# Kernel tuning notes

Hardware: AMD Instinct MI355X
Metric: run time of the kernel (lower is better)

Reference implementation:

```python
import jax, jax.numpy as jnp
import numpy as np

K = 3        # kernel_size
STRIDE = 1
PAD = 1
BASIS = 8    # act_fun.get_size()


def cheb_basis(x):
    """Chebyshev polynomial basis T_0..T_{BASIS-1} of tanh(x); appends basis axis."""
    t = jnp.tanh(x)
    polys = [jnp.ones_like(t), t]
    for _ in range(BASIS - 2):
        polys.append(2.0 * t * polys[-1] - polys[-2])
    return jnp.stack(polys, axis=-1)  # (..., BASIS)


def silu(x):
    return x * jax.nn.sigmoid(x)


def unfold(x):
    """torch F.unfold equivalent: (b,c,h,w) -> (b, c, K*K, L), L = ho*wo."""
    b, c, h, w = x.shape
    ho = (h - K + 2 * PAD) // STRIDE + 1
    wo = (w - K + 2 * PAD) // STRIDE + 1
    xp = jnp.pad(x, ((0, 0), (0, 0), (PAD, PAD), (PAD, PAD)))
    pats = [xp[:, :, i:i + STRIDE * ho:STRIDE, j:j + STRIDE * wo:STRIDE]
            for i in range(K) for j in range(K)]
    pats = jnp.stack(pats, axis=2)  # (b, c, K*K, ho, wo)
    return pats.reshape(b, c, K * K, ho * wo), ho, wo


def setup_inputs() -> dict:
    key = jax.random.key(0)
    k1, k2, k3 = jax.random.split(key, 3)
    cin, cout = 64, 64
    x = jax.random.normal(k1, (16, cin, 32, 32), dtype=jnp.float32)
    # xavier_normal_ on (in,out,k^2,1): std = sqrt(2/(fan_in+fan_out)) approx
    w = jax.random.normal(k2, (cin, cout, K * K), dtype=jnp.float32) * jnp.sqrt(2.0 / (cin + cout))
    # normal_(c, 0, 0.1) on (in,out,k^2,1,basis) -> squeeze the broadcast dim
    c = jax.random.normal(k3, (cin, cout, K * K, BASIS), dtype=jnp.float32) * 0.1
    return {"x": x, "w": w, "c": c}


def reference(x, w, c):
    b = x.shape[0]
    pats, ho, wo = unfold(x)          # (b, i, k, l)
    res = silu(pats)                  # residual activation path
    act = cheb_basis(pats)            # (b, i, k, l, s) spline basis
    # sum_i sum_k w[i,o,k] * res[b,i,k,l]
    term1 = jnp.einsum('iok,bikl->bol', w, res)
    # sum_i sum_k sum_s w[i,o,k]*c[i,o,k,s]*act[b,i,k,l,s] (fused, avoids (b,i,o,k,l,s))
    cw = c * w[..., None]             # (i, o, k, s)
    term2 = jnp.einsum('ioks,bikls->bol', cw, act)
    return (term1 + term2).reshape(b, -1, ho, wo)
```

## Files before the change

kernel.cpp:

```cpp
#include <hip/hip_runtime.h>
#include <hip/hip_bf16.h>


#define CIN   64
#define COUT  64
#define HW    32
#define LL    1024
#define NS    8

typedef __attribute__((ext_vector_type(8))) short short8;
typedef __attribute__((ext_vector_type(16))) float f32x16;


__global__ void prep_kernel(const float* __restrict__ w,
                            const float* __restrict__ c,
                            __hip_bfloat16* __restrict__ Wt,
                            float* __restrict__ bias,
                            const float* __restrict__ x,
                            float* __restrict__ dummy) {
    const int bx = blockIdx.x;
    if (bx < 144) {
        const int tid = bx * 256 + threadIdx.x;
        const int i = tid / (9 * COUT);
        const int r = tid - i * 9 * COUT;
        const int k = r / COUT;
        const int o = r - k * COUT;
        const int widx = (i * COUT + o) * 9 + k;
        const float wv = w[widx];
        __hip_bfloat16* dst = Wt + (size_t)tid * NS;
        dst[0] = __float2bfloat16(wv);
#pragma unroll
        for (int s = 1; s < 8; ++s) dst[s] = __float2bfloat16(wv * c[widx * 8 + s]);
        return;
    }
    if (bx < 208) {
        const int o = bx - 144;
        const int i = threadIdx.x;
        if (i >= 64) return;
        float v = 0.f;
#pragma unroll
        for (int k = 0; k < 9; ++k) {
            const int idx = (i * COUT + o) * 9 + k;
            v += w[idx] * c[idx * 8];
        }
#pragma unroll
        for (int off = 32; off > 0; off >>= 1) v += __shfl_down(v, off);
        if (i == 0) bias[o] = v;
        return;
    }
    const int idx = bx - 208;
    const int r  = idx & 7;
    const int m  = idx >> 3;
    const int b  = r + 8 * (m & 1);
    const int ch = m >> 1;
    const float4 v = ((const float4*)(x + (size_t)(b * CIN + ch) * LL))[threadIdx.x];
    const float acc = v.x + v.y + v.z + v.w;
    if (acc == 1.0e-37f) dummy[threadIdx.x] = acc;
}

__global__ __launch_bounds__(1024, 4) void kan_fused_kernel(
        const float* __restrict__ x,
        const __hip_bfloat16* __restrict__ Wt,
        const float* __restrict__ bias,
        float* __restrict__ out) {
    __shared__ __align__(16) unsigned short Wlds[52224];

    const int tid  = threadIdx.x;
    const int wv   = tid >> 6;
    const int lane = tid & 63;
    const int l31  = lane & 31;
    const int half = lane >> 5;
    const int kq   = wv >> 1;
    const int om   = wv & 1;

    const int b    = blockIdx.x;
    const int row0 = blockIdx.y << 1;

    const unsigned short* WtU = (const unsigned short*)Wt;
    float* xf = (float*)Wlds;

#pragma unroll
    for (int p = 0; p < 9; ++p) {
        const int cell = p * 1024 + tid;
        if (cell < 8704) {
            const int ch  = cell / 136;
            const int pos = cell - ch * 136;
            const int r4  = pos / 34;
            const int col = pos - r4 * 34;
            const int gy  = row0 - 1 + r4;
            const int gx  = col - 1;
            float v = 0.f;
            if ((unsigned)gy < 32u && (unsigned)gx < 32u)
                v = x[((size_t)(b * CIN + ch) * HW + gy) * HW + gx];
            xf[cell] = v;
        }
    }
    __syncthreads();

    f32x16 acc0, acc1;
#pragma unroll
    for (int r = 0; r < 16; ++r) { acc0[r] = 0.f; acc1[r] = 0.f; }

    const size_t wlane = ((size_t)(kq * 8 + half) * 9 * 64 + om * 32 + l31) * 8;

    for (int chunk = 0; chunk < 4; ++chunk) {
        unsigned short* ubuf = Wlds + 17408 + (chunk & 1) * 17408;

        auto doCell = [&](int cell) {
            const int kqc = cell / 272;
            const int rr  = cell - kqc * 272;
            const int chl = rr & 1;
            const int pos = rr >> 1;
            const float xv = xf[(kqc * 8 + chunk * 2 + chl) * 136 + pos];
            const float e   = __expf(xv);
            const float sig = e * __builtin_amdgcn_rcpf(1.f + e);
            const float res = xv * sig;
            const float t   = 1.f - 2.f * __builtin_amdgcn_rcpf(__builtin_fmaf(e, e, 1.f));
            const float t2  = t + t;
            const float T2 = __builtin_fmaf(t2, t,  -1.f);
            const float T3 = __builtin_fmaf(t2, T2, -t);
            const float T4 = __builtin_fmaf(t2, T3, -T2);
            const float T5 = __builtin_fmaf(t2, T4, -T3);
            const float T6 = __builtin_fmaf(t2, T5, -T4);
            const float T7 = __builtin_fmaf(t2, T6, -T5);
            union { __hip_bfloat162 h2[4]; float4 f4; } U;
            U.h2[0] = __float22bfloat162_rn(make_float2(res, t));
            U.h2[1] = __float22bfloat162_rn(make_float2(T2, T3));
            U.h2[2] = __float22bfloat162_rn(make_float2(T4, T5));
            U.h2[3] = __float22bfloat162_rn(make_float2(T6, T7));
            *(float4*)(ubuf + cell * 8) = U.f4;
        };
        doCell(tid);
        doCell(tid + 1024);
        if (tid < 128) doCell(tid + 2048);

        __syncthreads();

        const unsigned short* afb = ubuf + kq * 2176;
        const unsigned short* wc  = WtU + wlane + (size_t)chunk * 9216;
#pragma unroll
        for (int kpos = 0; kpos < 9; ++kpos) {
            const int posb = (kpos / 3) * 34 + (kpos % 3);
            short8 af0 = *(const short8*)(afb + ((posb      + l31) * 2 + half) * 8);
            short8 af1 = *(const short8*)(afb + ((posb + 34 + l31) * 2 + half) * 8);
            short8 wf  = *(const short8*)(wc + kpos * 512);
            acc0 = __builtin_amdgcn_mfma_f32_32x32x16_bf16(wf, af0, acc0, 0, 0, 0);
            acc1 = __builtin_amdgcn_mfma_f32_32x32x16_bf16(wf, af1, acc1, 0, 0, 0);
        }
    }

    float* red = (float*)Wlds;
#pragma unroll
    for (int h = 0; h < 2; ++h) {
        if (h) __syncthreads();
        if (om == h) {
#pragma unroll
            for (int r = 0; r < 16; ++r) {
                const int ol = (r & 3) + 8 * (r >> 2) + 4 * half;
                red[(kq * 64 +      l31) * 33 + ol] = acc0[r];
                red[(kq * 64 + 32 + l31) * 33 + ol] = acc1[r];
            }
        }
        __syncthreads();
#pragma unroll
        for (int rep = 0; rep < 2; ++rep) {
            const int v  = rep * 1024 + tid;
            const int p  = v & 63;
            const int ol = v >> 6;
            float s = bias[h * 32 + ol];
#pragma unroll
            for (int kqq = 0; kqq < 8; ++kqq)
                s += red[(kqq * 64 + p) * 33 + ol];
            out[(size_t)(b * COUT + h * 32 + ol) * LL + (row0 + (p >> 5)) * HW + (p & 31)] = s;
        }
    }
}

extern "C" void kernel_launch(void* const* d_in, const int* in_sizes, int n_in,
                              void* d_out, int out_size, void* d_ws, size_t ws_size,
                              hipStream_t stream) {
    const float* x = (const float*)d_in[0];
    const float* w = (const float*)d_in[1];
    const float* c = (const float*)d_in[2];
    float* out = (float*)d_out;

    char* ws = (char*)d_ws;
    __hip_bfloat16* Wt    = (__hip_bfloat16*)(ws);
    float*          bias  = (float*)(ws + 589824);
    float*          dummy = (float*)(ws + 590080);

    prep_kernel<<<1232, 256, 0, stream>>>(w, c, Wt, bias, x, dummy);
    kan_fused_kernel<<<dim3(16, 16), 1024, 0, stream>>>(x, Wt, bias, out);
}
```

Before: 74.92 us.

## Split output channels across blocks and prefetch input per chunk from global

Each block now handles one half of the output channels with 512 threads, doubling the grid, instead of 1024 threads covering both halves. The full x tile is no longer staged in LDS. Each thread loads its cells straight from global memory, prefetching the next chunk's values into registers while the current chunk is processed. The activation buffer layout changes so each half-wave reads contiguous entries, and MFMA issue priority is raised. The basis activations are now computed twice (once per output half), which adds ALU work in exchange for smaller blocks, less LDS and more blocks per device.

```diff
diff --git a/kernel.cpp b/kernel.cpp
--- a/kernel.cpp
+++ b/kernel.cpp
@@ -58,121 +58,129 @@
     if (acc == 1.0e-37f) dummy[threadIdx.x] = acc;
 }
 
-__global__ __launch_bounds__(1024, 4) void kan_fused_kernel(
+__global__ __launch_bounds__(512, 4) void kan_fused_kernel(
         const float* __restrict__ x,
         const __hip_bfloat16* __restrict__ Wt,
         const float* __restrict__ bias,
         float* __restrict__ out) {
-    __shared__ __align__(16) unsigned short Wlds[52224];
+    __shared__ __align__(16) unsigned short Wlds[34816];
 
     const int tid  = threadIdx.x;
-    const int wv   = tid >> 6;
+    const int kq   = tid >> 6;
     const int lane = tid & 63;
     const int l31  = lane & 31;
     const int half = lane >> 5;
-    const int kq   = wv >> 1;
-    const int om   = wv & 1;
-
-    const int b    = blockIdx.x;
+
+    const int bx   = blockIdx.x;
+    const int b    = bx >> 1;
+    const int oh   = bx & 1;
     const int row0 = blockIdx.y << 1;
 
     const unsigned short* WtU = (const unsigned short*)Wt;
-    float* xf = (float*)Wlds;
-
-#pragma unroll
-    for (int p = 0; p < 9; ++p) {
-        const int cell = p * 1024 + tid;
-        if (cell < 8704) {
-            const int ch  = cell / 136;
-            const int pos = cell - ch * 136;
-            const int r4  = pos / 34;
-            const int col = pos - r4 * 34;
-            const int gy  = row0 - 1 + r4;
-            const int gx  = col - 1;
-            float v = 0.f;
-            if ((unsigned)gy < 32u && (unsigned)gx < 32u)
-                v = x[((size_t)(b * CIN + ch) * HW + gy) * HW + gx];
-            xf[cell] = v;
-        }
-    }
-    __syncthreads();
+
+    int    cellv[5];
+    bool   liv[5];
+    bool   vld[5];
+    size_t xoff[5];
+#pragma unroll
+    for (int p = 0; p < 5; ++p) {
+        const int cell = p * 512 + tid;
+        const bool live = (p < 4) || (tid < 128);
+        const int g   = cell / 136;
+        const int pos = cell - g * 136;
+        const int r4  = pos / 34;
+        const int col = pos - r4 * 34;
+        const int gy  = row0 - 1 + r4;
+        const int gx  = col - 1;
+        cellv[p] = cell;
+        liv[p]   = live;
+        vld[p]   = live && ((unsigned)gy < 32u) && ((unsigned)gx < 32u);
+        const int ch0 = (g >> 1) * 8 + (g & 1);
+        xoff[p]  = ((size_t)(b * CIN + ch0) * HW + gy) * HW + gx;
+    }
 
     f32x16 acc0, acc1;
 #pragma unroll
     for (int r = 0; r < 16; ++r) { acc0[r] = 0.f; acc1[r] = 0.f; }
 
-    const size_t wlane = ((size_t)(kq * 8 + half) * 9 * 64 + om * 32 + l31) * 8;
+    const size_t wlane = ((size_t)(kq * 8 + half) * 9 * COUT + oh * 32 + l31) * NS;
+
+    float xc[5], xn[5];
+#pragma unroll
+    for (int p = 0; p < 5; ++p) xc[p] = vld[p] ? x[xoff[p]] : 0.f;
 
     for (int chunk = 0; chunk < 4; ++chunk) {
-        unsigned short* ubuf = Wlds + 17408 + (chunk & 1) * 17408;
-
-        auto doCell = [&](int cell) {
-            const int kqc = cell / 272;
-            const int rr  = cell - kqc * 272;
-            const int chl = rr & 1;
-            const int pos = rr >> 1;
-            const float xv = xf[(kqc * 8 + chunk * 2 + chl) * 136 + pos];
-            const float e   = __expf(xv);
-            const float sig = e * __builtin_amdgcn_rcpf(1.f + e);
-            const float res = xv * sig;
-            const float t   = 1.f - 2.f * __builtin_amdgcn_rcpf(__builtin_fmaf(e, e, 1.f));
-            const float t2  = t + t;
-            const float T2 = __builtin_fmaf(t2, t,  -1.f);
-            const float T3 = __builtin_fmaf(t2, T2, -t);
-            const float T4 = __builtin_fmaf(t2, T3, -T2);
-            const float T5 = __builtin_fmaf(t2, T4, -T3);
-            const float T6 = __builtin_fmaf(t2, T5, -T4);
-            const float T7 = __builtin_fmaf(t2, T6, -T5);
-            union { __hip_bfloat162 h2[4]; float4 f4; } U;
-            U.h2[0] = __float22bfloat162_rn(make_float2(res, t));
-            U.h2[1] = __float22bfloat162_rn(make_float2(T2, T3));
-            U.h2[2] = __float22bfloat162_rn(make_float2(T4, T5));
-            U.h2[3] = __float22bfloat162_rn(make_float2(T6, T7));
-            *(float4*)(ubuf + cell * 8) = U.f4;
-        };
-        doCell(tid);
-        doCell(tid + 1024);
-        if (tid < 128) doCell(tid + 2048);
-
+        unsigned short* ubuf = Wlds + (chunk & 1) * 17408;
+
+        if (chunk < 3) {
+#pragma unroll
+            for (int p = 0; p < 5; ++p)
+                xn[p] = vld[p] ? x[xoff[p] + (size_t)(chunk + 1) * 2 * HW * HW] : 0.f;
+        }
+
+#pragma unroll
+        for (int p = 0; p < 5; ++p) {
+            if (liv[p]) {
+                const float xv  = xc[p];
+                const float e   = __expf(xv);
+                const float sig = e * __builtin_amdgcn_rcpf(1.f + e);
+                const float res = xv * sig;
+                const float t   = 1.f - 2.f * __builtin_amdgcn_rcpf(__builtin_fmaf(e, e, 1.f));
+                const float t2  = t + t;
+                const float T2 = __builtin_fmaf(t2, t,  -1.f);
+                const float T3 = __builtin_fmaf(t2, T2, -t);
+                const float T4 = __builtin_fmaf(t2, T3, -T2);
+                const float T5 = __builtin_fmaf(t2, T4, -T3);
+                const float T6 = __builtin_fmaf(t2, T5, -T4);
+                const float T7 = __builtin_fmaf(t2, T6, -T5);
+                union { __hip_bfloat162 h2[4]; float4 f4; } U;
+                U.h2[0] = __float22bfloat162_rn(make_float2(res, t));
+                U.h2[1] = __float22bfloat162_rn(make_float2(T2, T3));
+                U.h2[2] = __float22bfloat162_rn(make_float2(T4, T5));
+                U.h2[3] = __float22bfloat162_rn(make_float2(T6, T7));
+                *(float4*)(ubuf + cellv[p] * 8) = U.f4;
+            }
+        }
         __syncthreads();
 
-        const unsigned short* afb = ubuf + kq * 2176;
+        const unsigned short* afb = ubuf + (kq * 2 + half) * 1088;
         const unsigned short* wc  = WtU + wlane + (size_t)chunk * 9216;
+        __builtin_amdgcn_s_setprio(1);
 #pragma unroll
         for (int kpos = 0; kpos < 9; ++kpos) {
             const int posb = (kpos / 3) * 34 + (kpos % 3);
-            short8 af0 = *(const short8*)(afb + ((posb      + l31) * 2 + half) * 8);
-            short8 af1 = *(const short8*)(afb + ((posb + 34 + l31) * 2 + half) * 8);
+            short8 af0 = *(const short8*)(afb + (posb      + l31) * 8);
+            short8 af1 = *(const short8*)(afb + (posb + 34 + l31) * 8);
             short8 wf  = *(const short8*)(wc + kpos * 512);
             acc0 = __builtin_amdgcn_mfma_f32_32x32x16_bf16(wf, af0, acc0, 0, 0, 0);
             acc1 = __builtin_amdgcn_mfma_f32_32x32x16_bf16(wf, af1, acc1, 0, 0, 0);
         }
-    }
-
+        __builtin_amdgcn_s_setprio(0);
+
+#pragma unroll
+        for (int p = 0; p < 5; ++p) xc[p] = xn[p];
+    }
+
+    __syncthreads();
     float* red = (float*)Wlds;
 #pragma unroll
-    for (int h = 0; h < 2; ++h) {
-        if (h) __syncthreads();
-        if (om == h) {
-#pragma unroll
-            for (int r = 0; r < 16; ++r) {
-                const int ol = (r & 3) + 8 * (r >> 2) + 4 * half;
-                red[(kq * 64 +      l31) * 33 + ol] = acc0[r];
-                red[(kq * 64 + 32 + l31) * 33 + ol] = acc1[r];
-            }
-        }
-        __syncthreads();
-#pragma unroll
-        for (int rep = 0; rep < 2; ++rep) {
-            const int v  = rep * 1024 + tid;
-            const int p  = v & 63;
-            const int ol = v >> 6;
-            float s = bias[h * 32 + ol];
-#pragma unroll
-            for (int kqq = 0; kqq < 8; ++kqq)
-                s += red[(kqq * 64 + p) * 33 + ol];
-            out[(size_t)(b * COUT + h * 32 + ol) * LL + (row0 + (p >> 5)) * HW + (p & 31)] = s;
-        }
+    for (int r = 0; r < 16; ++r) {
+        const int ol = (r & 3) + 8 * (r >> 2) + 4 * half;
+        red[(kq * 64 +      l31) * 33 + ol] = acc0[r];
+        red[(kq * 64 + 32 + l31) * 33 + ol] = acc1[r];
+    }
+    __syncthreads();
+
+#pragma unroll
+    for (int rep = 0; rep < 4; ++rep) {
+        const int v  = rep * 512 + tid;
+        const int p  = v & 63;
+        const int ol = v >> 6;
+        float s = bias[oh * 32 + ol];
+#pragma unroll
+        for (int kqq = 0; kqq < 8; ++kqq)
+            s += red[(kqq * 64 + p) * 33 + ol];
+        out[(size_t)(b * COUT + oh * 32 + ol) * LL + (row0 + (p >> 5)) * HW + (p & 31)] = s;
     }
 }
 
@@ -190,5 +198,5 @@
     float*          dummy = (float*)(ws + 590080);
 
     prep_kernel<<<1232, 256, 0, stream>>>(w, c, Wt, bias, x, dummy);
-    kan_fused_kernel<<<dim3(16, 16), 1024, 0, stream>>>(x, Wt, bias, out);
+    kan_fused_kernel<<<dim3(32, 16), 512, 0, stream>>>(x, Wt, bias, out);
 }
```

After: 78.02 us. +4.1%, slower.

## Merge prep and main kernels into one cooperative launch with grid sync

Applied to the files above, without the earlier changes.

Folds the weight/bias preprocessing and the x cache-warming pass into the main KAN kernel, launched cooperatively with 256 blocks and separated by a grid-wide barrier. This removes one kernel launch and the gap between dependent launches. In exchange every block pays for a grid sync, and the cooperative launch limits how blocks are scheduled. The prep work is now spread across all 256 blocks instead of 1232 smaller ones.

```diff
diff --git a/kernel.cpp b/kernel.cpp
--- a/kernel.cpp
+++ b/kernel.cpp
@@ -1,5 +1,8 @@
 #include <hip/hip_runtime.h>
 #include <hip/hip_bf16.h>
+#include <hip/hip_cooperative_groups.h>
+
+namespace cg = cooperative_groups;
 
 
 #define CIN   64
@@ -12,31 +15,34 @@
 typedef __attribute__((ext_vector_type(16))) float f32x16;
 
 
-__global__ void prep_kernel(const float* __restrict__ w,
-                            const float* __restrict__ c,
-                            __hip_bfloat16* __restrict__ Wt,
-                            float* __restrict__ bias,
-                            const float* __restrict__ x,
-                            float* __restrict__ dummy) {
-    const int bx = blockIdx.x;
-    if (bx < 144) {
-        const int tid = bx * 256 + threadIdx.x;
-        const int i = tid / (9 * COUT);
-        const int r = tid - i * 9 * COUT;
+__global__ __launch_bounds__(1024, 4) void kan_all_kernel(
+        const float* __restrict__ x,
+        const float* __restrict__ w,
+        const float* __restrict__ c,
+        __hip_bfloat16* __restrict__ Wt,
+        float* __restrict__ bias,
+        float* __restrict__ out) {
+    __shared__ __align__(16) unsigned short Wlds[52224];
+
+    const int tid = threadIdx.x;
+    const int bid = blockIdx.x;
+
+    if (tid < 144) {
+        const int e = bid * 144 + tid;
+        const int i = e / (9 * COUT);
+        const int r = e - i * 9 * COUT;
         const int k = r / COUT;
         const int o = r - k * COUT;
         const int widx = (i * COUT + o) * 9 + k;
-        const float wv = w[widx];
-        __hip_bfloat16* dst = Wt + (size_t)tid * NS;
-        dst[0] = __float2bfloat16(wv);
+        const float wval = w[widx];
+        __hip_bfloat16* dst = Wt + (size_t)e * NS;
+        dst[0] = __float2bfloat16(wval);
 #pragma unroll
-        for (int s = 1; s < 8; ++s) dst[s] = __float2bfloat16(wv * c[widx * 8 + s]);
-        return;
+        for (int s = 1; s < 8; ++s) dst[s] = __float2bfloat16(wval * c[widx * 8 + s]);
     }
-    if (bx < 208) {
-        const int o = bx - 144;
-        const int i = threadIdx.x;
-        if (i >= 64) return;
+    if (bid < 64 && tid < 64) {
+        const int o = bid;
+        const int i = tid;
         float v = 0.f;
 #pragma unroll
         for (int k = 0; k < 9; ++k) {
@@ -46,35 +52,24 @@
 #pragma unroll
         for (int off = 32; off > 0; off >>= 1) v += __shfl_down(v, off);
         if (i == 0) bias[o] = v;
-        return;
     }
-    const int idx = bx - 208;
-    const int r  = idx & 7;
-    const int m  = idx >> 3;
-    const int b  = r + 8 * (m & 1);
-    const int ch = m >> 1;
-    const float4 v = ((const float4*)(x + (size_t)(b * CIN + ch) * LL))[threadIdx.x];
-    const float acc = v.x + v.y + v.z + v.w;
-    if (acc == 1.0e-37f) dummy[threadIdx.x] = acc;
-}
+    {
+        const float4 v = ((const float4*)x)[bid * 1024 + tid];
+        const float a = v.x + v.y + v.z + v.w;
+        __asm__ volatile("" :: "v"(a));
+    }
 
-__global__ __launch_bounds__(1024, 4) void kan_fused_kernel(
-        const float* __restrict__ x,
-        const __hip_bfloat16* __restrict__ Wt,
-        const float* __restrict__ bias,
-        float* __restrict__ out) {
-    __shared__ __align__(16) unsigned short Wlds[52224];
+    cg::this_grid().sync();
 
-    const int tid  = threadIdx.x;
-    const int wv   = tid >> 6;
+    const int wvid = tid >> 6;
     const int lane = tid & 63;
     const int l31  = lane & 31;
     const int half = lane >> 5;
-    const int kq   = wv >> 1;
-    const int om   = wv & 1;
+    const int kq   = wvid >> 1;
+    const int om   = wvid & 1;
 
-    const int b    = blockIdx.x;
-    const int row0 = blockIdx.y << 1;
+    const int b    = bid >> 4;
+    const int row0 = (bid & 15) << 1;
 
     const unsigned short* WtU = (const unsigned short*)Wt;
     float* xf = (float*)Wlds;
@@ -101,7 +96,7 @@
 #pragma unroll
     for (int r = 0; r < 16; ++r) { acc0[r] = 0.f; acc1[r] = 0.f; }
 
-    const size_t wlane = ((size_t)(kq * 8 + half) * 9 * 64 + om * 32 + l31) * 8;
+    const size_t wlane = ((size_t)(kq * 8 + half) * 9 * COUT + om * 32 + l31) * NS;
 
     for (int chunk = 0; chunk < 4; ++chunk) {
         unsigned short* ubuf = Wlds + 17408 + (chunk & 1) * 17408;
@@ -185,10 +180,10 @@
     float* out = (float*)d_out;
 
     char* ws = (char*)d_ws;
-    __hip_bfloat16* Wt    = (__hip_bfloat16*)(ws);
-    float*          bias  = (float*)(ws + 589824);
-    float*          dummy = (float*)(ws + 590080);
+    __hip_bfloat16* Wt   = (__hip_bfloat16*)(ws);
+    float*          bias = (float*)(ws + 589824);
 
-    prep_kernel<<<1232, 256, 0, stream>>>(w, c, Wt, bias, x, dummy);
-    kan_fused_kernel<<<dim3(16, 16), 1024, 0, stream>>>(x, Wt, bias, out);
+    void* args[] = {(void*)&x, (void*)&w, (void*)&c, (void*)&Wt, (void*)&bias, (void*)&out};
+    hipLaunchCooperativeKernel((void*)kan_all_kernel, dim3(256), dim3(1024),
+                               args, 0, stream);
 }
```

Result: slower. 123.8 us (+65.2%).
